# Kernel tuning notes

Hardware: AMD Instinct MI355X
Metric: run time of the kernel (lower is better)

Reference implementation:

```python
import jax, jax.numpy as jnp
import numpy as np

NEG_SLOPE = 0.2  # PyG GATConv default negative_slope


def gat_conv(x, src, dst, num_nodes, W, att_src, att_dst, bias, heads, out_ch, concat):
    """PyG-style GATConv (eval mode, self-loops already included in src/dst).
    x: [N, in]; W: [in, heads*out_ch]; att_*: [heads, out_ch]; bias: [heads*out_ch] or [out_ch].
    """
    N = num_nodes
    h = (x @ W).reshape(N, heads, out_ch)                      # [N, H, C]
    a_src = jnp.sum(h * att_src[None], axis=-1)                 # [N, H]
    a_dst = jnp.sum(h * att_dst[None], axis=-1)                 # [N, H]
    e = a_src[src] + a_dst[dst]                                 # [E, H]
    e = jnp.where(e > 0, e, NEG_SLOPE * e)                      # leaky_relu
    # segment softmax over incoming edges of each destination node
    m = jax.ops.segment_max(e, dst, num_segments=N)             # [N, H]
    w = jnp.exp(e - m[dst])                                     # [E, H]
    denom = jax.ops.segment_sum(w, dst, num_segments=N)         # [N, H]
    alpha = w / denom[dst]                                      # [E, H]
    out = jax.ops.segment_sum(h[src] * alpha[:, :, None], dst, num_segments=N)  # [N, H, C]
    if concat:
        out = out.reshape(N, heads * out_ch)
    else:
        out = out.mean(axis=1)
    return out + bias


def setup_inputs() -> dict:
    key = jax.random.key(0)
    ks = jax.random.split(key, 20)
    N, T, F_IN = 100000, 50, 10
    E = 1600000
    H1, C1 = 4, 32          # conv1: heads=4, hidden=32 -> 128
    LAT = 64                # latent_dim

    def g(k, shape, scale):
        return (jax.random.normal(k, shape, dtype=jnp.float32) * scale)

    inp = {
        "temporal_data": jax.random.normal(ks[0], (N, T, F_IN), dtype=jnp.float32),
        "x": jax.random.normal(ks[1], (N, F_IN), dtype=jnp.float32),
        "edge_index": jax.random.randint(ks[2], (2, E), 0, N, dtype=jnp.int32),
        # temporal encoder: Linear(10,64) -> ReLU -> Linear(64,64)
        "tW1": g(ks[3], (F_IN, 64), 0.3), "tb1": jnp.zeros((64,), jnp.float32),
        "tW2": g(ks[4], (64, LAT), 0.12), "tb2": jnp.zeros((LAT,), jnp.float32),
        # GATConv1: in=10, out=32, heads=4, concat
        "gW1": g(ks[5], (F_IN, H1 * C1), 0.3),
        "ga1_src": g(ks[6], (H1, C1), 0.17), "ga1_dst": g(ks[7], (H1, C1), 0.17),
        "gb1": jnp.zeros((H1 * C1,), jnp.float32),
        # GATConv2: in=128, out=64, heads=1, concat=False
        "gW2": g(ks[8], (H1 * C1, LAT), 0.09),
        "ga2_src": g(ks[9], (1, LAT), 0.12), "ga2_dst": g(ks[10], (1, LAT), 0.12),
        "gb2": jnp.zeros((LAT,), jnp.float32),
        # classifier: Linear(128,64) -> ReLU -> (Dropout eval) -> Linear(64,1) -> Sigmoid
        "cW1": g(ks[11], (2 * LAT, 64), 0.09), "cb1": jnp.zeros((64,), jnp.float32),
        "cW2": g(ks[12], (64, 1), 0.12), "cb2": jnp.zeros((1,), jnp.float32),
    }
    return inp


def reference(temporal_data, x, edge_index, tW1, tb1, tW2, tb2,
              gW1, ga1_src, ga1_dst, gb1, gW2, ga2_src, ga2_dst, gb2,
              cW1, cb1, cW2, cb2):
    N = x.shape[0]
    # temporal encoder then mean over time axis (dim=1)
    t = jax.nn.relu(temporal_data @ tW1 + tb1) @ tW2 + tb2      # [N, T, 64]
    t = t.mean(axis=1)                                           # [N, 64]
    # add self-loops (PyG GATConv default add_self_loops=True)
    loop = jnp.arange(N, dtype=edge_index.dtype)
    src = jnp.concatenate([edge_index[0], loop])
    dst = jnp.concatenate([edge_index[1], loop])
    h = gat_conv(x, src, dst, N, gW1, ga1_src, ga1_dst, gb1, heads=4, out_ch=32, concat=True)
    h = jax.nn.elu(h)
    g = gat_conv(h, src, dst, N, gW2, ga2_src, ga2_dst, gb2, heads=1, out_ch=64, concat=False)  # [N, 64]
    combined = jnp.concatenate([t, g], axis=-1)                  # [N, 128]
    z = jax.nn.relu(combined @ cW1 + cb1) @ cW2 + cb2            # [N, 1]
    return jax.nn.sigmoid(z)
```

## Files before the change

### kernel.cpp

```cpp
#include <hip/hip_runtime.h>
#include <hip/hip_bf16.h>

#define DEV_INLINE __device__ __forceinline__

typedef __attribute__((ext_vector_type(8))) short short8v;
typedef __attribute__((ext_vector_type(4))) float f32x4;

DEV_INLINE float lrelu(float v) { return fmaxf(v, 0.2f * v); }

DEV_INLINE unsigned int cvt_pk_bf16(float lo, float hi) {
    unsigned int r;
    asm("v_cvt_pk_bf16_f32 %0, %1, %2" : "=v"(r) : "v"(lo), "v"(hi));
    return r;
}

DEV_INLINE unsigned short f2bf_rne(float f) {
    unsigned int b = __float_as_uint(f);
    return (unsigned short)((b + 0x7FFFu + ((b >> 16) & 1u)) >> 16);
}

DEV_INLINE unsigned int pack_bf16(float lo, float hi) {
    return (unsigned int)f2bf_rne(lo) | ((unsigned int)f2bf_rne(hi) << 16);
}

DEV_INLINE float bf_lo(unsigned int u) { return __uint_as_float(u << 16); }
DEV_INLINE float bf_hi(unsigned int u) { return __uint_as_float(u & 0xFFFF0000u); }

__global__ __launch_bounds__(1024) void k_scan1(const int* __restrict__ counts,
                                                int* __restrict__ rowptr,
                                                int* __restrict__ partials, int N) {
    __shared__ int sd[1024];
    int li = threadIdx.x;
    int i  = blockIdx.x * 1024 + li;
    int v  = (i < N) ? counts[i] : 0;
    sd[li] = v;
    __syncthreads();
    for (int off = 1; off < 1024; off <<= 1) {
        int t = (li >= off) ? sd[li - off] : 0;
        __syncthreads();
        sd[li] += t;
        __syncthreads();
    }
    int inc = sd[li];
    if (i < N) rowptr[i + 1] = inc;
    if (li == 1023) partials[blockIdx.x] = inc;
}

__global__ void k_scan3(int* __restrict__ rowptr, const int* __restrict__ partials,
                        int* __restrict__ nxt, int N) {
    int i = blockIdx.x * blockDim.x + threadIdx.x;
    if (i > N) return;
    int v;
    if (i == 0) { v = 0; rowptr[0] = 0; }
    else {
        int blk = (i - 1) >> 10;
        int pp = 0;
        for (int b = 0; b < blk; ++b) pp += partials[b];
        v = rowptr[i] + pp;
        rowptr[i] = v;
    }
    if (i < N) nxt[i] = v;
}

#define SC_K 8
#define SC_P 16
__global__ __launch_bounds__(256) void k_scatter(const int* __restrict__ ei,
                                                 int* __restrict__ nxt,
                                                 int* __restrict__ col,
                                                 int E, int range) {
    int t = threadIdx.x;
    int base = blockIdx.x * (256 * SC_K);
    int s[SC_K], d[SC_K];
#pragma unroll
    for (int k = 0; k < SC_K; ++k) {
        int e = base + k * 256 + t;
        bool v = (e < E);
        s[k] = v ? ei[e] : 0;
        d[k] = v ? ei[E + e] : -1;
    }
    int lo = 0;
    for (int p = 0; p < SC_P; ++p, lo += range) {
        int hi = lo + range;
#pragma unroll
        for (int k = 0; k < SC_K; ++k) {
            if (d[k] >= lo && d[k] < hi) {
                int pos = atomicAdd(&nxt[d[k]], 1);
                col[pos] = s[k];
            }
        }
        __syncthreads();
    }
}

__global__ __launch_bounds__(256) void k_temporal(const float* __restrict__ td,
                                                  const float* __restrict__ tW1,
                                                  const float* __restrict__ tb1,
                                                  const int* __restrict__ ei,
                                                  int* __restrict__ counts,
                                                  const float* __restrict__ tW2,
                                                  const float* __restrict__ cW1,
                                                  const float* __restrict__ tb2,
                                                  const float* __restrict__ cb1,
                                                  unsigned short* __restrict__ Wf,
                                                  float* __restrict__ bcf,
                                                  unsigned short* __restrict__ mb,
                                                  int N, int E) {
    int tid = threadIdx.x, lane = tid & 63;
    int gid = blockIdx.x * 256 + tid;

    int estr = gridDim.x * 256;
    for (int e = gid; e < E; e += estr) atomicAdd(&counts[ei[E + e]], 1);

    if (gid < 4096) {
        int i = gid >> 6, c = gid & 63;
        float s = 0.f;
#pragma unroll 8
        for (int k = 0; k < 64; ++k) s = fmaf(tW2[i * 64 + k], cW1[k * 64 + c], s);
        Wf[gid] = f2bf_rne(s);
    } else if (gid < 8192) {
        Wf[gid] = f2bf_rne(cW1[gid]);
    } else if (gid < 8256) {
        int c = gid - 8192;
        float s = cb1[c];
#pragma unroll 8
        for (int k = 0; k < 64; ++k) s = fmaf(tb2[k], cW1[k * 64 + c], s);
        bcf[c] = s;
    }

    int wid  = gid >> 6;
    int nwav = (gridDim.x * 256) >> 6;
    int col  = lane & 15;
    int g    = lane >> 4;

    short8v B[4];
#pragma unroll
    for (int cb = 0; cb < 4; ++cb) {
        union { short8v v; unsigned short u[8]; } bu;
#pragma unroll
        for (int j = 0; j < 8; ++j) {
            int f = g * 8 + j;
            int c = cb * 16 + col;
            float w = (f < 10) ? tW1[f * 64 + c] : ((f == 10) ? tb1[c] : 0.f);
            bu.u[j] = f2bf_rne(w);
        }
        B[cb] = bu.v;
    }

    for (int n = wid; n < N; n += nwav) {
        const float* base = td + (size_t)n * 500;
        float sum0 = 0.f, sum1 = 0.f, sum2 = 0.f, sum3 = 0.f;
#pragma unroll
        for (int tt = 0; tt < 4; ++tt) {
            int t = tt * 16 + col;
            bool valid = (t < 50);
            float x0 = 0.f, x1 = 0.f, x2 = 0.f, x3 = 0.f;
            float x4 = 0.f, x5 = 0.f, x6 = 0.f, x7 = 0.f;
            const float* rp = base + t * 10;
            if (g == 0 && valid) {
                float2 p0 = *reinterpret_cast<const float2*>(rp);
                float2 p1 = *reinterpret_cast<const float2*>(rp + 2);
                float2 p2 = *reinterpret_cast<const float2*>(rp + 4);
                float2 p3 = *reinterpret_cast<const float2*>(rp + 6);
                x0 = p0.x; x1 = p0.y; x2 = p1.x; x3 = p1.y;
                x4 = p2.x; x5 = p2.y; x6 = p3.x; x7 = p3.y;
            } else if (g == 1 && valid) {
                float2 p4 = *reinterpret_cast<const float2*>(rp + 8);
                x0 = p4.x; x1 = p4.y; x2 = 1.0f;
            }
            union { short8v v; unsigned int w[4]; } au;
            au.w[0] = cvt_pk_bf16(x0, x1);
            au.w[1] = cvt_pk_bf16(x2, x3);
            au.w[2] = cvt_pk_bf16(x4, x5);
            au.w[3] = cvt_pk_bf16(x6, x7);

            f32x4 z = {0.f, 0.f, 0.f, 0.f};
            f32x4 c0 = __builtin_amdgcn_mfma_f32_16x16x32_bf16(au.v, B[0], z, 0, 0, 0);
            f32x4 c1 = __builtin_amdgcn_mfma_f32_16x16x32_bf16(au.v, B[1], z, 0, 0, 0);
            f32x4 c2 = __builtin_amdgcn_mfma_f32_16x16x32_bf16(au.v, B[2], z, 0, 0, 0);
            f32x4 c3 = __builtin_amdgcn_mfma_f32_16x16x32_bf16(au.v, B[3], z, 0, 0, 0);
#pragma unroll
            for (int i = 0; i < 4; ++i) {
                sum0 += fmaxf(c0[i], 0.f);
                sum1 += fmaxf(c1[i], 0.f);
                sum2 += fmaxf(c2[i], 0.f);
                sum3 += fmaxf(c3[i], 0.f);
            }
        }
        sum0 += __shfl_xor(sum0, 16); sum0 += __shfl_xor(sum0, 32);
        sum1 += __shfl_xor(sum1, 16); sum1 += __shfl_xor(sum1, 32);
        sum2 += __shfl_xor(sum2, 16); sum2 += __shfl_xor(sum2, 32);
        sum3 += __shfl_xor(sum3, 16); sum3 += __shfl_xor(sum3, 32);
        float mv = (g == 0) ? sum0 : (g == 1) ? sum1 : (g == 2) ? sum2 : sum3;
        mb[(size_t)n * 64 + lane] = f2bf_rne(mv * 0.02f);
    }
}

__global__ __launch_bounds__(256) void k_g1a(const float* __restrict__ x,
                                             const float* __restrict__ gW1,
                                             const float* __restrict__ as_w,
                                             const float* __restrict__ ad_w,
                                             unsigned short* __restrict__ h1b,
                                             float* __restrict__ a1s,
                                             float* __restrict__ a1d, int N) {
    int tid = threadIdx.x, lane = tid & 63;
    int n0 = blockIdx.x * 4 + (tid >> 6);
    int n  = __builtin_amdgcn_readfirstlane(n0 < N ? n0 : N - 1);

    float wa[10], wb[10];
#pragma unroll
    for (int i = 0; i < 10; ++i) { wa[i] = gW1[i * 128 + lane]; wb[i] = gW1[i * 128 + 64 + lane]; }
    const float* xp = x + (size_t)n * 10;
    float ha = 0.f, hb = 0.f;
#pragma unroll
    for (int i = 0; i < 10; ++i) { float xv = xp[i]; ha = fmaf(xv, wa[i], ha); hb = fmaf(xv, wb[i], hb); }

    int c = lane & 31;
    int headA = lane >> 5;
    float ps_a = ha * as_w[headA * 32 + c];
    float ps_b = hb * as_w[(headA + 2) * 32 + c];
    float pd_a = ha * ad_w[headA * 32 + c];
    float pd_b = hb * ad_w[(headA + 2) * 32 + c];
#pragma unroll
    for (int m = 1; m < 32; m <<= 1) {
        ps_a += __shfl_xor(ps_a, m); ps_b += __shfl_xor(ps_b, m);
        pd_a += __shfl_xor(pd_a, m); pd_b += __shfl_xor(pd_b, m);
    }
    if (n0 < N) {
        h1b[(size_t)n * 128 + lane]      = f2bf_rne(ha);
        h1b[(size_t)n * 128 + 64 + lane] = f2bf_rne(hb);
        if (c == 0) {
            a1s[n * 4 + headA]     = ps_a;
            a1s[n * 4 + 2 + headA] = ps_b;
            a1d[n * 4 + headA]     = pd_a;
            a1d[n * 4 + 2 + headA] = pd_b;
        }
    }
}

__global__ __launch_bounds__(256) void k_g1b(const int* __restrict__ rowptr,
                                             const int* __restrict__ col,
                                             const unsigned int* __restrict__ h1u,
                                             const float* __restrict__ a1s,
                                             const float* __restrict__ a1d,
                                             const float* __restrict__ gb1,
                                             unsigned int* __restrict__ out1u, int N) {
    int tid = threadIdx.x, lane = tid & 63;
    int n0 = blockIdx.x * 4 + (tid >> 6);
    int n  = __builtin_amdgcn_readfirstlane(n0 < N ? n0 : N - 1);

    int start = rowptr[n], end = rowptr[n + 1];
    int q = lane >> 4, c = lane & 15;
    int hsel = c >> 2;
    float advh = a1d[n * 4 + hsel];
    const uint4* h1q = reinterpret_cast<const uint4*>(h1u);

    float den = 0.f;
    float a0 = 0.f, a1v = 0.f, a2v = 0.f, a3v = 0.f;
    float a4 = 0.f, a5 = 0.f, a6 = 0.f, a7 = 0.f;
    if (q == 0) {
        float w = __expf(lrelu(a1s[n * 4 + hsel] + advh));
        uint4 u = h1q[(size_t)n * 16 + c];
        den = w;
        a0 = w * bf_lo(u.x); a1v = w * bf_hi(u.x);
        a2v = w * bf_lo(u.y); a3v = w * bf_hi(u.y);
        a4 = w * bf_lo(u.z); a5 = w * bf_hi(u.z);
        a6 = w * bf_lo(u.w); a7 = w * bf_hi(u.w);
    }
    int e = start + q;
    for (; e + 4 < end; e += 8) {
        int s0 = col[e], s1 = col[e + 4];
        float q0 = a1s[s0 * 4 + hsel];
        float q1 = a1s[s1 * 4 + hsel];
        uint4 u0 = h1q[(size_t)s0 * 16 + c];
        uint4 u1 = h1q[(size_t)s1 * 16 + c];
        float w0 = __expf(lrelu(q0 + advh));
        float w1 = __expf(lrelu(q1 + advh));
        den += w0 + w1;
        a0 = fmaf(w0, bf_lo(u0.x), a0); a1v = fmaf(w0, bf_hi(u0.x), a1v);
        a2v = fmaf(w0, bf_lo(u0.y), a2v); a3v = fmaf(w0, bf_hi(u0.y), a3v);
        a4 = fmaf(w0, bf_lo(u0.z), a4); a5 = fmaf(w0, bf_hi(u0.z), a5);
        a6 = fmaf(w0, bf_lo(u0.w), a6); a7 = fmaf(w0, bf_hi(u0.w), a7);
        a0 = fmaf(w1, bf_lo(u1.x), a0); a1v = fmaf(w1, bf_hi(u1.x), a1v);
        a2v = fmaf(w1, bf_lo(u1.y), a2v); a3v = fmaf(w1, bf_hi(u1.y), a3v);
        a4 = fmaf(w1, bf_lo(u1.z), a4); a5 = fmaf(w1, bf_hi(u1.z), a5);
        a6 = fmaf(w1, bf_lo(u1.w), a6); a7 = fmaf(w1, bf_hi(u1.w), a7);
    }
    if (e < end) {
        int s = col[e];
        float qv = a1s[s * 4 + hsel];
        uint4 u = h1q[(size_t)s * 16 + c];
        float w = __expf(lrelu(qv + advh));
        den += w;
        a0 = fmaf(w, bf_lo(u.x), a0); a1v = fmaf(w, bf_hi(u.x), a1v);
        a2v = fmaf(w, bf_lo(u.y), a2v); a3v = fmaf(w, bf_hi(u.y), a3v);
        a4 = fmaf(w, bf_lo(u.z), a4); a5 = fmaf(w, bf_hi(u.z), a5);
        a6 = fmaf(w, bf_lo(u.w), a6); a7 = fmaf(w, bf_hi(u.w), a7);
    }
#define RED2(v) v += __shfl_xor(v, 16); v += __shfl_xor(v, 32);
    RED2(den) RED2(a0) RED2(a1v) RED2(a2v) RED2(a3v)
    RED2(a4) RED2(a5) RED2(a6) RED2(a7)
#undef RED2

    if (n0 < N && lane < 16) {
        float inv = 1.f / den;
        float v0 = a0 * inv + gb1[8 * c + 0];
        float v1 = a1v * inv + gb1[8 * c + 1];
        float v2 = a2v * inv + gb1[8 * c + 2];
        float v3 = a3v * inv + gb1[8 * c + 3];
        float v4 = a4 * inv + gb1[8 * c + 4];
        float v5 = a5 * inv + gb1[8 * c + 5];
        float v6 = a6 * inv + gb1[8 * c + 6];
        float v7 = a7 * inv + gb1[8 * c + 7];
        v0 = (v0 > 0.f) ? v0 : (__expf(v0) - 1.f);
        v1 = (v1 > 0.f) ? v1 : (__expf(v1) - 1.f);
        v2 = (v2 > 0.f) ? v2 : (__expf(v2) - 1.f);
        v3 = (v3 > 0.f) ? v3 : (__expf(v3) - 1.f);
        v4 = (v4 > 0.f) ? v4 : (__expf(v4) - 1.f);
        v5 = (v5 > 0.f) ? v5 : (__expf(v5) - 1.f);
        v6 = (v6 > 0.f) ? v6 : (__expf(v6) - 1.f);
        v7 = (v7 > 0.f) ? v7 : (__expf(v7) - 1.f);
        uint4 o;
        o.x = pack_bf16(v0, v1); o.y = pack_bf16(v2, v3);
        o.z = pack_bf16(v4, v5); o.w = pack_bf16(v6, v7);
        *reinterpret_cast<uint4*>(out1u + (size_t)n * 64 + 4 * c) = o;
    }
}

__global__ __launch_bounds__(256) void k_g2a(const unsigned short* __restrict__ out1b,
                                             const float* __restrict__ gW2,
                                             const float* __restrict__ a2sw,
                                             const float* __restrict__ a2dw,
                                             unsigned short* __restrict__ h2b,
                                             float* __restrict__ a2s,
                                             float* __restrict__ a2d, int N) {
    int lane = threadIdx.x & 63;
    int wid  = (blockIdx.x * blockDim.x + threadIdx.x) >> 6;
    int nwav = (gridDim.x * blockDim.x) >> 6;
    int col = lane & 15, g4 = lane >> 4;

    short8v Bf[4][4];
#pragma unroll
    for (int ks = 0; ks < 4; ++ks)
#pragma unroll
        for (int cb = 0; cb < 4; ++cb) {
            union { short8v v; unsigned short u[8]; } bu;
#pragma unroll
            for (int j = 0; j < 8; ++j)
                bu.u[j] = f2bf_rne(gW2[(ks * 32 + g4 * 8 + j) * 64 + cb * 16 + col]);
            Bf[ks][cb] = bu.v;
        }
    float asv[4], adv[4];
#pragma unroll
    for (int cb = 0; cb < 4; ++cb) { asv[cb] = a2sw[cb * 16 + col]; adv[cb] = a2dw[cb * 16 + col]; }

    int ntile = (N + 15) >> 4;
    for (int t = wid; t < ntile; t += nwav) {
        int n0 = t * 16;
        int node = n0 + col; if (node >= N) node = N - 1;
        const unsigned short* xr = out1b + (size_t)node * 128;
        f32x4 acc0 = {0.f, 0.f, 0.f, 0.f}, acc1 = acc0, acc2 = acc0, acc3 = acc0;
#pragma unroll
        for (int ks = 0; ks < 4; ++ks) {
            short8v a = *reinterpret_cast<const short8v*>(xr + ks * 32 + g4 * 8);
            acc0 = __builtin_amdgcn_mfma_f32_16x16x32_bf16(a, Bf[ks][0], acc0, 0, 0, 0);
            acc1 = __builtin_amdgcn_mfma_f32_16x16x32_bf16(a, Bf[ks][1], acc1, 0, 0, 0);
            acc2 = __builtin_amdgcn_mfma_f32_16x16x32_bf16(a, Bf[ks][2], acc2, 0, 0, 0);
            acc3 = __builtin_amdgcn_mfma_f32_16x16x32_bf16(a, Bf[ks][3], acc3, 0, 0, 0);
        }
        float ps[4] = {0.f, 0.f, 0.f, 0.f}, pd[4] = {0.f, 0.f, 0.f, 0.f};
#define G2A_EPI(CB, ACC)                                                      \
        {                                                                     \
            _Pragma("unroll")                                                 \
            for (int i = 0; i < 4; ++i) {                                     \
                float v = ACC[i];                                             \
                int r = n0 + g4 * 4 + i;                                      \
                if (r < N) h2b[(size_t)r * 64 + CB * 16 + col] = f2bf_rne(v); \
                ps[i] = fmaf(v, asv[CB], ps[i]);                              \
                pd[i] = fmaf(v, adv[CB], pd[i]);                              \
            }                                                                 \
        }
        G2A_EPI(0, acc0) G2A_EPI(1, acc1) G2A_EPI(2, acc2) G2A_EPI(3, acc3)
#undef G2A_EPI
#pragma unroll
        for (int i = 0; i < 4; ++i) {
            ps[i] += __shfl_xor(ps[i], 1); ps[i] += __shfl_xor(ps[i], 2);
            ps[i] += __shfl_xor(ps[i], 4); ps[i] += __shfl_xor(ps[i], 8);
            pd[i] += __shfl_xor(pd[i], 1); pd[i] += __shfl_xor(pd[i], 2);
            pd[i] += __shfl_xor(pd[i], 4); pd[i] += __shfl_xor(pd[i], 8);
        }
        if (col == 0) {
#pragma unroll
            for (int i = 0; i < 4; ++i) {
                int r = n0 + g4 * 4 + i;
                if (r < N) { a2s[r] = ps[i]; a2d[r] = pd[i]; }
            }
        }
    }
}

__global__ __launch_bounds__(256) void k_g2b(const int* __restrict__ rowptr,
                                             const int* __restrict__ col,
                                             const unsigned int* __restrict__ h2u,
                                             const float* __restrict__ a2s,
                                             const float* __restrict__ a2d,
                                             const float* __restrict__ gb2,
                                             unsigned int* __restrict__ gu, int N) {
    int tid = threadIdx.x, lane = tid & 63;
    int n0 = blockIdx.x * 4 + (tid >> 6);
    int n  = __builtin_amdgcn_readfirstlane(n0 < N ? n0 : N - 1);

    int start = rowptr[n], end = rowptr[n + 1];
    int q = lane >> 3, c = lane & 7;
    float ad = a2d[n];
    const uint4* h2q = reinterpret_cast<const uint4*>(h2u);

    float den = 0.f;
    float a0 = 0.f, a1v = 0.f, a2v = 0.f, a3v = 0.f;
    float a4 = 0.f, a5 = 0.f, a6 = 0.f, a7 = 0.f;
    if (q == 0) {
        float w = __expf(lrelu(a2s[n] + ad));
        uint4 u = h2q[(size_t)n * 8 + c];
        den = w;
        a0 = w * bf_lo(u.x); a1v = w * bf_hi(u.x);
        a2v = w * bf_lo(u.y); a3v = w * bf_hi(u.y);
        a4 = w * bf_lo(u.z); a5 = w * bf_hi(u.z);
        a6 = w * bf_lo(u.w); a7 = w * bf_hi(u.w);
    }
    for (int e = start + q; e < end; e += 8) {
        int s = col[e];
        float w = __expf(lrelu(a2s[s] + ad));
        uint4 u = h2q[(size_t)s * 8 + c];
        den += w;
        a0 = fmaf(w, bf_lo(u.x), a0); a1v = fmaf(w, bf_hi(u.x), a1v);
        a2v = fmaf(w, bf_lo(u.y), a2v); a3v = fmaf(w, bf_hi(u.y), a3v);
        a4 = fmaf(w, bf_lo(u.z), a4); a5 = fmaf(w, bf_hi(u.z), a5);
        a6 = fmaf(w, bf_lo(u.w), a6); a7 = fmaf(w, bf_hi(u.w), a7);
    }
#define RED3(v) v += __shfl_xor(v, 8); v += __shfl_xor(v, 16); v += __shfl_xor(v, 32);
    RED3(den) RED3(a0) RED3(a1v) RED3(a2v) RED3(a3v)
    RED3(a4) RED3(a5) RED3(a6) RED3(a7)
#undef RED3

    if (n0 < N && lane < 8) {
        float inv = 1.f / den;
        uint4 o;
        o.x = pack_bf16(a0 * inv + gb2[8 * c + 0], a1v * inv + gb2[8 * c + 1]);
        o.y = pack_bf16(a2v * inv + gb2[8 * c + 2], a3v * inv + gb2[8 * c + 3]);
        o.z = pack_bf16(a4 * inv + gb2[8 * c + 4], a5 * inv + gb2[8 * c + 5]);
        o.w = pack_bf16(a6 * inv + gb2[8 * c + 6], a7 * inv + gb2[8 * c + 7]);
        *reinterpret_cast<uint4*>(gu + (size_t)n * 32 + 4 * c) = o;
    }
}

__global__ __launch_bounds__(256) void k_cls(const unsigned short* __restrict__ mb,
                                             const unsigned short* __restrict__ gb,
                                             const unsigned short* __restrict__ Wf,
                                             const float* __restrict__ bc,
                                             const float* __restrict__ cW2,
                                             const float* __restrict__ cb2,
                                             float* __restrict__ out, int N) {
    int lane = threadIdx.x & 63;
    int wid  = (blockIdx.x * blockDim.x + threadIdx.x) >> 6;
    int nwav = (gridDim.x * blockDim.x) >> 6;
    int col = lane & 15, g4 = lane >> 4;

    short8v Bf[4][4];
#pragma unroll
    for (int ks = 0; ks < 4; ++ks)
#pragma unroll
        for (int cb = 0; cb < 4; ++cb) {
            union { short8v v; unsigned short u[8]; } bu;
#pragma unroll
            for (int j = 0; j < 8; ++j)
                bu.u[j] = Wf[(ks * 32 + g4 * 8 + j) * 64 + cb * 16 + col];
            Bf[ks][cb] = bu.v;
        }
    float w2v[4], bcv[4];
#pragma unroll
    for (int cb = 0; cb < 4; ++cb) { w2v[cb] = cW2[cb * 16 + col]; bcv[cb] = bc[cb * 16 + col]; }
    float cb2v = cb2[0];

    int ntile = (N + 15) >> 4;
    for (int t = wid; t < ntile; t += nwav) {
        int n0 = t * 16;
        int node = n0 + col; if (node >= N) node = N - 1;
        const unsigned short* mr = mb + (size_t)node * 64;
        const unsigned short* gr = gb + (size_t)node * 64;
        f32x4 acc0 = {0.f, 0.f, 0.f, 0.f}, acc1 = acc0, acc2 = acc0, acc3 = acc0;
#pragma unroll
        for (int ks = 0; ks < 4; ++ks) {
            short8v a = (ks < 2)
                ? *reinterpret_cast<const short8v*>(mr + ks * 32 + g4 * 8)
                : *reinterpret_cast<const short8v*>(gr + (ks - 2) * 32 + g4 * 8);
            acc0 = __builtin_amdgcn_mfma_f32_16x16x32_bf16(a, Bf[ks][0], acc0, 0, 0, 0);
            acc1 = __builtin_amdgcn_mfma_f32_16x16x32_bf16(a, Bf[ks][1], acc1, 0, 0, 0);
            acc2 = __builtin_amdgcn_mfma_f32_16x16x32_bf16(a, Bf[ks][2], acc2, 0, 0, 0);
            acc3 = __builtin_amdgcn_mfma_f32_16x16x32_bf16(a, Bf[ks][3], acc3, 0, 0, 0);
        }
        float z[4] = {0.f, 0.f, 0.f, 0.f};
#define CLS_EPI(CB, ACC)                                                   \
        {                                                                  \
            _Pragma("unroll")                                              \
            for (int i = 0; i < 4; ++i)                                    \
                z[i] = fmaf(fmaxf(ACC[i] + bcv[CB], 0.f), w2v[CB], z[i]);  \
        }
        CLS_EPI(0, acc0) CLS_EPI(1, acc1) CLS_EPI(2, acc2) CLS_EPI(3, acc3)
#undef CLS_EPI
#pragma unroll
        for (int i = 0; i < 4; ++i) {
            z[i] += __shfl_xor(z[i], 1); z[i] += __shfl_xor(z[i], 2);
            z[i] += __shfl_xor(z[i], 4); z[i] += __shfl_xor(z[i], 8);
        }
        if (col == 0) {
#pragma unroll
            for (int i = 0; i < 4; ++i) {
                int r = n0 + g4 * 4 + i;
                if (r < N) out[r] = 1.f / (1.f + __expf(-(z[i] + cb2v)));
            }
        }
    }
}

extern "C" void kernel_launch(void* const* d_in, const int* in_sizes, int n_in,
                              void* d_out, int out_size, void* d_ws, size_t ws_size,
                              hipStream_t stream) {
    const float* td   = (const float*)d_in[0];
    const float* x    = (const float*)d_in[1];
    const int*   ei   = (const int*)d_in[2];
    const float* tW1  = (const float*)d_in[3];
    const float* tb1  = (const float*)d_in[4];
    const float* tW2  = (const float*)d_in[5];
    const float* tb2  = (const float*)d_in[6];
    const float* gW1  = (const float*)d_in[7];
    const float* ga1s = (const float*)d_in[8];
    const float* ga1d = (const float*)d_in[9];
    const float* gb1  = (const float*)d_in[10];
    const float* gW2  = (const float*)d_in[11];
    const float* ga2s = (const float*)d_in[12];
    const float* ga2d = (const float*)d_in[13];
    const float* gb2  = (const float*)d_in[14];
    const float* cW1  = (const float*)d_in[15];
    const float* cb1  = (const float*)d_in[16];
    const float* cW2  = (const float*)d_in[17];
    const float* cb2  = (const float*)d_in[18];

    int N = in_sizes[1] / 10;
    int E = in_sizes[2] / 2;

    float* fws = (float*)d_ws;
    unsigned short* mb16   = (unsigned short*)fws;
    unsigned short* h1b    = (unsigned short*)(fws + (size_t)N * 32);
    unsigned short* out1b  = (unsigned short*)(fws + (size_t)N * 96);
    float* a1s   = fws + (size_t)N * 160;
    float* a1d   = fws + (size_t)N * 164;
    unsigned short* h2b = h1b;
    float* a2s   = a1s;
    float* a2d   = a1d;
    unsigned short* gb16 = out1b;

    int* ib       = (int*)(fws + (size_t)N * 168);
    int* counts   = ib;
    int* rowptr   = ib + N;
    int* nxt      = ib + 2 * N + 1;
    int* partials = ib + 3 * N + 1;
    int* col      = ib + 3 * N + 1 + 128;

    unsigned short* Wf = (unsigned short*)(col + E);
    float* bcf = (float*)(Wf + 8192);

    hipMemsetAsync(counts, 0, (size_t)N * sizeof(int), stream);

    int NB = (N + 1023) / 1024;
    int range = (N + SC_P - 1) / SC_P;
    int nb4   = (N + 3) / 4;
    int ntile = (N + 15) / 16;
    int nbt   = (ntile + 3) / 4;

    k_temporal<<<2048, 256, 0, stream>>>(td, tW1, tb1, ei, counts,
                                         tW2, cW1, tb2, cb1, Wf, bcf, mb16, N, E);
    k_scan1  <<<NB, 1024, 0, stream>>>(counts, rowptr, partials, N);
    k_scan3  <<<(N + 1 + 255) / 256, 256, 0, stream>>>(rowptr, partials, nxt, N);
    k_scatter<<<(E + 256 * SC_K - 1) / (256 * SC_K), 256, 0, stream>>>(ei, nxt, col, E, range);

    k_g1a<<<nb4, 256, 0, stream>>>(x, gW1, ga1s, ga1d, h1b, a1s, a1d, N);
    k_g1b<<<nb4, 256, 0, stream>>>(rowptr, col, (const unsigned int*)h1b, a1s, a1d, gb1,
                                   (unsigned int*)out1b, N);
    k_g2a<<<nbt, 256, 0, stream>>>(out1b, gW2, ga2s, ga2d, h2b, a2s, a2d, N);
    k_g2b<<<nb4, 256, 0, stream>>>(rowptr, col, (const unsigned int*)h2b, a2s, a2d, gb2,
                                   (unsigned int*)gb16, N);
    k_cls<<<nbt, 256, 0, stream>>>(mb16, gb16, Wf, bcf, cW2, cb2, (float*)d_out, N);
}
```

Baseline: 420.1 us.

## Stage temporal rows through per-wave LDS double buffer with register prefetch

The temporal encoder now gives each wave a contiguous chunk of nodes instead of a strided loop. Each node's 500-float row is loaded with coalesced float4 reads into a per-wave LDS double buffer, and rows two to four nodes ahead are prefetched into registers. The goal is to replace the scattered float2 global loads with coalesced bulk loads and to hide memory latency behind the MFMA work. In exchange it uses 16KB of LDS per block, which may limit occupancy. It also has no explicit wave-level barrier between the LDS writes and reads, so it relies on in-wave ordering.

```diff
diff --git a/kernel.cpp b/kernel.cpp
--- a/kernel.cpp
+++ b/kernel.cpp
@@ -92,6 +92,54 @@
     }
 }
 
+DEV_INLINE void temporal_node(const float* wb, int col, int g, const short8v* B,
+                              int lane, unsigned short* mb, size_t n) {
+    float sum0 = 0.f, sum1 = 0.f, sum2 = 0.f, sum3 = 0.f;
+#pragma unroll
+    for (int tt = 0; tt < 4; ++tt) {
+        int t = tt * 16 + col;
+        bool valid = (t < 50);
+        float x0 = 0.f, x1 = 0.f, x2 = 0.f, x3 = 0.f;
+        float x4 = 0.f, x5 = 0.f, x6 = 0.f, x7 = 0.f;
+        const float* rp = wb + t * 10;
+        if (g == 0 && valid) {
+            float2 p0 = *reinterpret_cast<const float2*>(rp);
+            float2 p1 = *reinterpret_cast<const float2*>(rp + 2);
+            float2 p2 = *reinterpret_cast<const float2*>(rp + 4);
+            float2 p3 = *reinterpret_cast<const float2*>(rp + 6);
+            x0 = p0.x; x1 = p0.y; x2 = p1.x; x3 = p1.y;
+            x4 = p2.x; x5 = p2.y; x6 = p3.x; x7 = p3.y;
+        } else if (g == 1 && valid) {
+            float2 p4 = *reinterpret_cast<const float2*>(rp + 8);
+            x0 = p4.x; x1 = p4.y; x2 = 1.0f;
+        }
+        union { short8v v; unsigned int w[4]; } au;
+        au.w[0] = cvt_pk_bf16(x0, x1);
+        au.w[1] = cvt_pk_bf16(x2, x3);
+        au.w[2] = cvt_pk_bf16(x4, x5);
+        au.w[3] = cvt_pk_bf16(x6, x7);
+
+        f32x4 z = {0.f, 0.f, 0.f, 0.f};
+        f32x4 c0 = __builtin_amdgcn_mfma_f32_16x16x32_bf16(au.v, B[0], z, 0, 0, 0);
+        f32x4 c1 = __builtin_amdgcn_mfma_f32_16x16x32_bf16(au.v, B[1], z, 0, 0, 0);
+        f32x4 c2 = __builtin_amdgcn_mfma_f32_16x16x32_bf16(au.v, B[2], z, 0, 0, 0);
+        f32x4 c3 = __builtin_amdgcn_mfma_f32_16x16x32_bf16(au.v, B[3], z, 0, 0, 0);
+#pragma unroll
+        for (int i = 0; i < 4; ++i) {
+            sum0 += fmaxf(c0[i], 0.f);
+            sum1 += fmaxf(c1[i], 0.f);
+            sum2 += fmaxf(c2[i], 0.f);
+            sum3 += fmaxf(c3[i], 0.f);
+        }
+    }
+    sum0 += __shfl_xor(sum0, 16); sum0 += __shfl_xor(sum0, 32);
+    sum1 += __shfl_xor(sum1, 16); sum1 += __shfl_xor(sum1, 32);
+    sum2 += __shfl_xor(sum2, 16); sum2 += __shfl_xor(sum2, 32);
+    sum3 += __shfl_xor(sum3, 16); sum3 += __shfl_xor(sum3, 32);
+    float mv = (g == 0) ? sum0 : (g == 1) ? sum1 : (g == 2) ? sum2 : sum3;
+    mb[n * 64 + lane] = f2bf_rne(mv * 0.02f);
+}
+
 __global__ __launch_bounds__(256) void k_temporal(const float* __restrict__ td,
                                                   const float* __restrict__ tW1,
                                                   const float* __restrict__ tb1,
@@ -105,7 +153,8 @@
                                                   float* __restrict__ bcf,
                                                   unsigned short* __restrict__ mb,
                                                   int N, int E) {
-    int tid = threadIdx.x, lane = tid & 63;
+    __shared__ float lds[4][2][512];
+    int tid = threadIdx.x, lane = tid & 63, wv = tid >> 6;
     int gid = blockIdx.x * 256 + tid;
 
     int estr = gridDim.x * 256;
@@ -132,6 +181,12 @@
     int col  = lane & 15;
     int g    = lane >> 4;
 
+    int chunk = (N + nwav - 1) / nwav;
+    int n0 = wid * chunk;
+    int n1 = min(n0 + chunk, N);
+    if (n0 >= n1) return;
+    int cnt = n1 - n0;
+
     short8v B[4];
 #pragma unroll
     for (int cb = 0; cb < 4; ++cb) {
@@ -146,52 +201,57 @@
         B[cb] = bu.v;
     }
 
-    for (int n = wid; n < N; n += nwav) {
-        const float* base = td + (size_t)n * 500;
-        float sum0 = 0.f, sum1 = 0.f, sum2 = 0.f, sum3 = 0.f;
-#pragma unroll
-        for (int tt = 0; tt < 4; ++tt) {
-            int t = tt * 16 + col;
-            bool valid = (t < 50);
-            float x0 = 0.f, x1 = 0.f, x2 = 0.f, x3 = 0.f;
-            float x4 = 0.f, x5 = 0.f, x6 = 0.f, x7 = 0.f;
-            const float* rp = base + t * 10;
-            if (g == 0 && valid) {
-                float2 p0 = *reinterpret_cast<const float2*>(rp);
-                float2 p1 = *reinterpret_cast<const float2*>(rp + 2);
-                float2 p2 = *reinterpret_cast<const float2*>(rp + 4);
-                float2 p3 = *reinterpret_cast<const float2*>(rp + 6);
-                x0 = p0.x; x1 = p0.y; x2 = p1.x; x3 = p1.y;
-                x4 = p2.x; x5 = p2.y; x6 = p3.x; x7 = p3.y;
-            } else if (g == 1 && valid) {
-                float2 p4 = *reinterpret_cast<const float2*>(rp + 8);
-                x0 = p4.x; x1 = p4.y; x2 = 1.0f;
+    float* buf0 = &lds[wv][0][0];
+    float* buf1 = &lds[wv][1][0];
+
+    auto rowp = [&](int j) {
+        int n = n0 + j; if (n > n1 - 1) n = n1 - 1;
+        return reinterpret_cast<const float4*>(td + (size_t)n * 500);
+    };
+
+    float4 zero4 = make_float4(0.f, 0.f, 0.f, 0.f);
+    {
+        const float4* r0 = rowp(0);
+        float4 a = r0[lane];
+        float4 b = (lane < 61) ? r0[64 + lane] : zero4;
+        *reinterpret_cast<float4*>(buf0 + 4 * lane) = a;
+        if (lane < 61) *reinterpret_cast<float4*>(buf0 + 256 + 4 * lane) = b;
+        const float4* r1 = rowp(1);
+        a = r1[lane];
+        b = (lane < 61) ? r1[64 + lane] : zero4;
+        *reinterpret_cast<float4*>(buf1 + 4 * lane) = a;
+        if (lane < 61) *reinterpret_cast<float4*>(buf1 + 256 + 4 * lane) = b;
+    }
+    const float4* r2 = rowp(2);
+    float4 aA = r2[lane];
+    float4 bA = (lane < 61) ? r2[64 + lane] : zero4;
+    const float4* r3 = rowp(3);
+    float4 aB = r3[lane];
+    float4 bB = (lane < 61) ? r3[64 + lane] : zero4;
+
+    for (int i = 0; i < cnt; ++i) {
+        float* wb = (i & 1) ? buf1 : buf0;
+        temporal_node(wb, col, g, B, lane, mb, (size_t)(n0 + i));
+
+        if (i + 2 < cnt) {
+            if (i & 1) {
+                *reinterpret_cast<float4*>(buf1 + 4 * lane) = aB;
+                if (lane < 61) *reinterpret_cast<float4*>(buf1 + 256 + 4 * lane) = bB;
+            } else {
+                *reinterpret_cast<float4*>(buf0 + 4 * lane) = aA;
+                if (lane < 61) *reinterpret_cast<float4*>(buf0 + 256 + 4 * lane) = bA;
             }
-            union { short8v v; unsigned int w[4]; } au;
-            au.w[0] = cvt_pk_bf16(x0, x1);
-            au.w[1] = cvt_pk_bf16(x2, x3);
-            au.w[2] = cvt_pk_bf16(x4, x5);
-            au.w[3] = cvt_pk_bf16(x6, x7);
-
-            f32x4 z = {0.f, 0.f, 0.f, 0.f};
-            f32x4 c0 = __builtin_amdgcn_mfma_f32_16x16x32_bf16(au.v, B[0], z, 0, 0, 0);
-            f32x4 c1 = __builtin_amdgcn_mfma_f32_16x16x32_bf16(au.v, B[1], z, 0, 0, 0);
-            f32x4 c2 = __builtin_amdgcn_mfma_f32_16x16x32_bf16(au.v, B[2], z, 0, 0, 0);
-            f32x4 c3 = __builtin_amdgcn_mfma_f32_16x16x32_bf16(au.v, B[3], z, 0, 0, 0);
-#pragma unroll
-            for (int i = 0; i < 4; ++i) {
-                sum0 += fmaxf(c0[i], 0.f);
-                sum1 += fmaxf(c1[i], 0.f);
-                sum2 += fmaxf(c2[i], 0.f);
-                sum3 += fmaxf(c3[i], 0.f);
+        }
+        if (i + 4 < cnt) {
+            const float4* rn = reinterpret_cast<const float4*>(td + (size_t)(n0 + i + 4) * 500);
+            if (i & 1) {
+                aB = rn[lane];
+                if (lane < 61) bB = rn[64 + lane];
+            } else {
+                aA = rn[lane];
+                if (lane < 61) bA = rn[64 + lane];
             }
         }
-        sum0 += __shfl_xor(sum0, 16); sum0 += __shfl_xor(sum0, 32);
-        sum1 += __shfl_xor(sum1, 16); sum1 += __shfl_xor(sum1, 32);
-        sum2 += __shfl_xor(sum2, 16); sum2 += __shfl_xor(sum2, 32);
-        sum3 += __shfl_xor(sum3, 16); sum3 += __shfl_xor(sum3, 32);
-        float mv = (g == 0) ? sum0 : (g == 1) ? sum1 : (g == 2) ? sum2 : sum3;
-        mb[(size_t)n * 64 + lane] = f2bf_rne(mv * 0.02f);
     }
 }
 
```

Result: no change. 421.5 us (+0.3%).

## Stage temporal rows through LDS with coalesced float4 loads and double buffering

Applied to the files above, without the earlier changes.

The temporal encoder stops reading each node's 500-float row with scattered per-lane float2 global loads. Each wave now loads whole rows with coalesced float4 loads into registers, prefetches a few rows ahead, and double-buffers them in per-wave LDS before running the MFMA computation from LDS. Nodes are assigned to waves in contiguous chunks instead of a grid stride. This aims to hide global memory latency and improve coalescing, at the cost of extra LDS traffic and register use, and a chunked split that may balance load worse. There is no barrier between the per-wave LDS writes and reads, so correctness relies on wave-level ordering.

```diff
diff --git a/kernel.cpp b/kernel.cpp
--- a/kernel.cpp
+++ b/kernel.cpp
@@ -92,6 +92,54 @@
     }
 }
 
+DEV_INLINE void temporal_node(const float* wb, int col, int g, const short8v* B,
+                              int lane, unsigned short* mb, size_t n) {
+    float sum0 = 0.f, sum1 = 0.f, sum2 = 0.f, sum3 = 0.f;
+#pragma unroll
+    for (int tt = 0; tt < 4; ++tt) {
+        int t = tt * 16 + col;
+        bool valid = (t < 50);
+        float x0 = 0.f, x1 = 0.f, x2 = 0.f, x3 = 0.f;
+        float x4 = 0.f, x5 = 0.f, x6 = 0.f, x7 = 0.f;
+        const float* rp = wb + t * 10;
+        if (g == 0 && valid) {
+            float2 p0 = *reinterpret_cast<const float2*>(rp);
+            float2 p1 = *reinterpret_cast<const float2*>(rp + 2);
+            float2 p2 = *reinterpret_cast<const float2*>(rp + 4);
+            float2 p3 = *reinterpret_cast<const float2*>(rp + 6);
+            x0 = p0.x; x1 = p0.y; x2 = p1.x; x3 = p1.y;
+            x4 = p2.x; x5 = p2.y; x6 = p3.x; x7 = p3.y;
+        } else if (g == 1 && valid) {
+            float2 p4 = *reinterpret_cast<const float2*>(rp + 8);
+            x0 = p4.x; x1 = p4.y; x2 = 1.0f;
+        }
+        union { short8v v; unsigned int w[4]; } au;
+        au.w[0] = cvt_pk_bf16(x0, x1);
+        au.w[1] = cvt_pk_bf16(x2, x3);
+        au.w[2] = cvt_pk_bf16(x4, x5);
+        au.w[3] = cvt_pk_bf16(x6, x7);
+
+        f32x4 z = {0.f, 0.f, 0.f, 0.f};
+        f32x4 c0 = __builtin_amdgcn_mfma_f32_16x16x32_bf16(au.v, B[0], z, 0, 0, 0);
+        f32x4 c1 = __builtin_amdgcn_mfma_f32_16x16x32_bf16(au.v, B[1], z, 0, 0, 0);
+        f32x4 c2 = __builtin_amdgcn_mfma_f32_16x16x32_bf16(au.v, B[2], z, 0, 0, 0);
+        f32x4 c3 = __builtin_amdgcn_mfma_f32_16x16x32_bf16(au.v, B[3], z, 0, 0, 0);
+#pragma unroll
+        for (int i = 0; i < 4; ++i) {
+            sum0 += fmaxf(c0[i], 0.f);
+            sum1 += fmaxf(c1[i], 0.f);
+            sum2 += fmaxf(c2[i], 0.f);
+            sum3 += fmaxf(c3[i], 0.f);
+        }
+    }
+    sum0 += __shfl_xor(sum0, 16); sum0 += __shfl_xor(sum0, 32);
+    sum1 += __shfl_xor(sum1, 16); sum1 += __shfl_xor(sum1, 32);
+    sum2 += __shfl_xor(sum2, 16); sum2 += __shfl_xor(sum2, 32);
+    sum3 += __shfl_xor(sum3, 16); sum3 += __shfl_xor(sum3, 32);
+    float mv = (g == 0) ? sum0 : (g == 1) ? sum1 : (g == 2) ? sum2 : sum3;
+    mb[n * 64 + lane] = f2bf_rne(mv * 0.02f);
+}
+
 __global__ __launch_bounds__(256) void k_temporal(const float* __restrict__ td,
                                                   const float* __restrict__ tW1,
                                                   const float* __restrict__ tb1,
@@ -105,7 +153,9 @@
                                                   float* __restrict__ bcf,
                                                   unsigned short* __restrict__ mb,
                                                   int N, int E) {
-    int tid = threadIdx.x, lane = tid & 63;
+    __shared__ float b0lds[4][512];
+    __shared__ float b1lds[4][512];
+    int tid = threadIdx.x, lane = tid & 63, wv = tid >> 6;
     int gid = blockIdx.x * 256 + tid;
 
     int estr = gridDim.x * 256;
@@ -132,6 +182,12 @@
     int col  = lane & 15;
     int g    = lane >> 4;
 
+    int chunk = (N + nwav - 1) / nwav;
+    int n0 = wid * chunk;
+    int n1 = min(n0 + chunk, N);
+    if (n0 >= n1) return;
+    int cnt = n1 - n0;
+
     short8v B[4];
 #pragma unroll
     for (int cb = 0; cb < 4; ++cb) {
@@ -146,53 +202,44 @@
         B[cb] = bu.v;
     }
 
-    for (int n = wid; n < N; n += nwav) {
-        const float* base = td + (size_t)n * 500;
-        float sum0 = 0.f, sum1 = 0.f, sum2 = 0.f, sum3 = 0.f;
-#pragma unroll
-        for (int tt = 0; tt < 4; ++tt) {
-            int t = tt * 16 + col;
-            bool valid = (t < 50);
-            float x0 = 0.f, x1 = 0.f, x2 = 0.f, x3 = 0.f;
-            float x4 = 0.f, x5 = 0.f, x6 = 0.f, x7 = 0.f;
-            const float* rp = base + t * 10;
-            if (g == 0 && valid) {
-                float2 p0 = *reinterpret_cast<const float2*>(rp);
-                float2 p1 = *reinterpret_cast<const float2*>(rp + 2);
-                float2 p2 = *reinterpret_cast<const float2*>(rp + 4);
-                float2 p3 = *reinterpret_cast<const float2*>(rp + 6);
-                x0 = p0.x; x1 = p0.y; x2 = p1.x; x3 = p1.y;
-                x4 = p2.x; x5 = p2.y; x6 = p3.x; x7 = p3.y;
-            } else if (g == 1 && valid) {
-                float2 p4 = *reinterpret_cast<const float2*>(rp + 8);
-                x0 = p4.x; x1 = p4.y; x2 = 1.0f;
-            }
-            union { short8v v; unsigned int w[4]; } au;
-            au.w[0] = cvt_pk_bf16(x0, x1);
-            au.w[1] = cvt_pk_bf16(x2, x3);
-            au.w[2] = cvt_pk_bf16(x4, x5);
-            au.w[3] = cvt_pk_bf16(x6, x7);
-
-            f32x4 z = {0.f, 0.f, 0.f, 0.f};
-            f32x4 c0 = __builtin_amdgcn_mfma_f32_16x16x32_bf16(au.v, B[0], z, 0, 0, 0);
-            f32x4 c1 = __builtin_amdgcn_mfma_f32_16x16x32_bf16(au.v, B[1], z, 0, 0, 0);
-            f32x4 c2 = __builtin_amdgcn_mfma_f32_16x16x32_bf16(au.v, B[2], z, 0, 0, 0);
-            f32x4 c3 = __builtin_amdgcn_mfma_f32_16x16x32_bf16(au.v, B[3], z, 0, 0, 0);
-#pragma unroll
-            for (int i = 0; i < 4; ++i) {
-                sum0 += fmaxf(c0[i], 0.f);
-                sum1 += fmaxf(c1[i], 0.f);
-                sum2 += fmaxf(c2[i], 0.f);
-                sum3 += fmaxf(c3[i], 0.f);
-            }
-        }
-        sum0 += __shfl_xor(sum0, 16); sum0 += __shfl_xor(sum0, 32);
-        sum1 += __shfl_xor(sum1, 16); sum1 += __shfl_xor(sum1, 32);
-        sum2 += __shfl_xor(sum2, 16); sum2 += __shfl_xor(sum2, 32);
-        sum3 += __shfl_xor(sum3, 16); sum3 += __shfl_xor(sum3, 32);
-        float mv = (g == 0) ? sum0 : (g == 1) ? sum1 : (g == 2) ? sum2 : sum3;
-        mb[(size_t)n * 64 + lane] = f2bf_rne(mv * 0.02f);
-    }
+    float* buf0 = &b0lds[wv][0];
+    float* buf1 = &b1lds[wv][0];
+    float4 zero4 = make_float4(0.f, 0.f, 0.f, 0.f);
+
+#define LOADROW(J, A, Bv)                                                      \
+    {                                                                          \
+        int nn = n0 + (J); if (nn > n1 - 1) nn = n1 - 1;                       \
+        const float4* rr = reinterpret_cast<const float4*>(td + (size_t)nn * 500); \
+        A = rr[lane];                                                          \
+        Bv = (lane < 61) ? rr[64 + lane] : zero4;                              \
+    }
+#define WRITEBUF(BUF, A, Bv)                                                   \
+    {                                                                          \
+        *reinterpret_cast<float4*>((BUF) + 4 * lane) = A;                      \
+        if (lane < 61) *reinterpret_cast<float4*>((BUF) + 256 + 4 * lane) = Bv;\
+    }
+
+    float4 aA, bA, aB, bB;
+    LOADROW(0, aA, bA)
+    LOADROW(1, aB, bB)
+    WRITEBUF(buf0, aA, bA)
+    LOADROW(2, aA, bA)
+    WRITEBUF(buf1, aB, bB)
+    LOADROW(3, aB, bB)
+
+    int i = 0;
+    for (; i + 1 < cnt; i += 2) {
+        temporal_node(buf0, col, g, B, lane, mb, (size_t)(n0 + i));
+        WRITEBUF(buf0, aA, bA)
+        LOADROW(i + 4, aA, bA)
+        temporal_node(buf1, col, g, B, lane, mb, (size_t)(n0 + i + 1));
+        WRITEBUF(buf1, aB, bB)
+        LOADROW(i + 5, aB, bB)
+    }
+    if (i < cnt)
+        temporal_node(buf0, col, g, B, lane, mb, (size_t)(n0 + i));
+#undef LOADROW
+#undef WRITEBUF
 }
 
 __global__ __launch_bounds__(256) void k_g1a(const float* __restrict__ x,
```

New measurement: 393.6 us. 1.07x faster.
